# Kernel tuning notes

Hardware: AMD Instinct MI355X
Metric: run time of the kernel (lower is better)

## Reference

```python
import jax, jax.numpy as jnp
import numpy as np

N = 12288
E = 393216
IN_DIM = 256

def _glorot(key, shape):
    lim = float(np.sqrt(6.0 / (shape[0] + shape[1])))
    return jax.random.uniform(key, shape, jnp.float32, -lim, lim)

def setup_inputs() -> dict:
    key = jax.random.key(0)
    ks = jax.random.split(key, 8)
    x = jax.random.normal(ks[0], (N, IN_DIM), jnp.float32)
    edge_index = jax.random.randint(ks[1], (2, E), 0, N, jnp.int64)
    params = {
        'W_e1': _glorot(ks[2], (IN_DIM, 128)), 'b_e1': jnp.zeros((128,), jnp.float32),
        'W_e2': _glorot(ks[3], (128, 64)),     'b_e2': jnp.zeros((64,), jnp.float32),
        'W_a1': _glorot(ks[4], (64, 128)),     'b_a1': jnp.zeros((128,), jnp.float32),
        'W_a2': _glorot(ks[5], (128, IN_DIM)), 'b_a2': jnp.zeros((IN_DIM,), jnp.float32),
        'W_s':  _glorot(ks[6], (64, 64)),      'b_s':  jnp.zeros((64,), jnp.float32),
    }
    return {'x': x, 'edge_index': edge_index, **params}

def _gcn(x, W, b, src, dst, deg_inv, norm):
    # GCNConv: D^{-1/2}(A+I)D^{-1/2} X W + b, self-loops added
    h = x @ W                                   # [N, F_out]
    agg = jax.ops.segment_sum(h[src] * norm[:, None], dst, num_segments=N)
    agg = agg + h * deg_inv[:, None]            # self-loop term (norm = 1/deg)
    return agg + b

def reference(x, edge_index, W_e1, b_e1, W_e2, b_e2, W_a1, b_a1, W_a2, b_a2, W_s, b_s):
    src, dst = edge_index[0], edge_index[1]
    deg = jnp.zeros((N,), jnp.float32).at[dst].add(1.0) + 1.0  # includes self-loop
    dinv_sqrt = jax.lax.rsqrt(deg)
    norm = dinv_sqrt[src] * dinv_sqrt[dst]      # per-edge norm [E]
    deg_inv = 1.0 / deg
    # Encoder
    h = jax.nn.relu(_gcn(x, W_e1, b_e1, src, dst, deg_inv, norm))
    z = jax.nn.relu(_gcn(h, W_e2, b_e2, src, dst, deg_inv, norm))
    # Attribute decoder
    a = jax.nn.relu(_gcn(z, W_a1, b_a1, src, dst, deg_inv, norm))
    x_hat = _gcn(a, W_a2, b_a2, src, dst, deg_inv, norm)
    # Structure decoder
    s = jax.nn.relu(_gcn(z, W_s, b_s, src, dst, deg_inv, norm))
    a_hat = s @ s.T                             # [N, N]
    return (x_hat, a_hat, z)
```

## Files before the change

### kernel.cpp

```cpp
#include <hip/hip_runtime.h>
#include <hip/hip_bf16.h>

#define N_NODES 12288
#define N_EDGES 393216

typedef __attribute__((ext_vector_type(8))) short bf16x8;
typedef __attribute__((ext_vector_type(4))) float f32x4;


__global__ __launch_bounds__(256) void detect_kernel(const unsigned* __restrict__ w,
                                                     unsigned* __restrict__ flag) {
  int i = blockIdx.x * 256 + threadIdx.x;
  unsigned v = w[2 * i + 1];
  unsigned long long b = __ballot(v != 0);
  if ((threadIdx.x & 63) == 0 && b) atomicOr(flag, 1u);
}


__global__ __launch_bounds__(256) void count_kernel(const int* __restrict__ ei,
                                                    const unsigned* __restrict__ flag,
                                                    int* __restrict__ cnt) {
  const bool wide = (*flag == 0);
  int e = blockIdx.x * 256 + threadIdx.x;
  int d = wide ? ei[2 * (N_EDGES + e)] : ei[N_EDGES + e];
  atomicAdd(&cnt[d], 1);
}

__global__ __launch_bounds__(1024) void scan_kernel(const int* __restrict__ cnt,
                                                    int* __restrict__ csr_off,
                                                    int* __restrict__ cursor,
                                                    float* __restrict__ dinv_sqrt,
                                                    float* __restrict__ deg_inv) {
  __shared__ int sdata[1024];
  const int tid = threadIdx.x;
  int carry = 0;
  for (int base = 0; base < N_NODES; base += 1024) {
    int i = base + tid;
    int c = (i < N_NODES) ? cnt[i] : 0;
    if (i < N_NODES) {
      float d = (float)(c + 1);
      dinv_sqrt[i] = rsqrtf(d);
      deg_inv[i] = 1.0f / d;
    }
    sdata[tid] = c;
    __syncthreads();
    for (int off = 1; off < 1024; off <<= 1) {
      int v = (tid >= off) ? sdata[tid - off] : 0;
      __syncthreads();
      sdata[tid] += v;
      __syncthreads();
    }
    int incl = sdata[tid];
    if (i < N_NODES) {
      int excl = carry + incl - c;
      csr_off[i] = excl;
      cursor[i] = excl;
    }
    int total = sdata[1023];
    __syncthreads();
    carry += total;
  }
  if (tid == 0) csr_off[N_NODES] = carry;
}

__global__ __launch_bounds__(256) void scatter_kernel(const int* __restrict__ ei,
                                                      const unsigned* __restrict__ flag,
                                                      const float* __restrict__ dinv_sqrt,
                                                      int* __restrict__ cursor,
                                                      int* __restrict__ csr_src,
                                                      float* __restrict__ csr_w) {
  const bool wide = (*flag == 0);
  int e = blockIdx.x * 256 + threadIdx.x;
  int s = wide ? ei[2 * e] : ei[e];
  int d = wide ? ei[2 * (N_EDGES + e)] : ei[N_EDGES + e];
  int p = atomicAdd(&cursor[d], 1);
  csr_src[p] = s;
  csr_w[p] = dinv_sqrt[s] * dinv_sqrt[d];
}


template <bool BIAS, bool RELU>
__global__ __launch_bounds__(256) void gemm_kernel(const float* __restrict__ A,
                                                   const float* __restrict__ B,
                                                   const float* __restrict__ bias,
                                                   float* __restrict__ C,
                                                   int K, int Nf) {
  __shared__ float As[16][65];
  __shared__ float Bs[16][68];
  const int tid = threadIdx.x;
  const int bm = blockIdx.y * 64;
  const int bn = blockIdx.x * 64;
  const int tr = (tid >> 4) * 4;
  const int tc = (tid & 15) * 4;
  const int lm = tid >> 2;
  const int lk = (tid & 3) * 4;
  const int lbk = tid >> 4;
  const int lbc = (tid & 15) * 4;
  float acc[4][4] = {};
  for (int k0 = 0; k0 < K; k0 += 16) {
    float4 a4 = *reinterpret_cast<const float4*>(&A[(size_t)(bm + lm) * K + k0 + lk]);
    float4 b4 = *reinterpret_cast<const float4*>(&B[(size_t)(k0 + lbk) * Nf + bn + lbc]);
    As[lk + 0][lm] = a4.x; As[lk + 1][lm] = a4.y; As[lk + 2][lm] = a4.z; As[lk + 3][lm] = a4.w;
    Bs[lbk][lbc + 0] = b4.x; Bs[lbk][lbc + 1] = b4.y; Bs[lbk][lbc + 2] = b4.z; Bs[lbk][lbc + 3] = b4.w;
    __syncthreads();
#pragma unroll
    for (int kk = 0; kk < 16; ++kk) {
      float av[4], bv[4];
#pragma unroll
      for (int i = 0; i < 4; ++i) av[i] = As[kk][tr + i];
#pragma unroll
      for (int j = 0; j < 4; ++j) bv[j] = Bs[kk][tc + j];
#pragma unroll
      for (int i = 0; i < 4; ++i)
#pragma unroll
        for (int j = 0; j < 4; ++j) acc[i][j] = fmaf(av[i], bv[j], acc[i][j]);
    }
    __syncthreads();
  }
#pragma unroll
  for (int i = 0; i < 4; ++i) {
    float v[4];
#pragma unroll
    for (int j = 0; j < 4; ++j) {
      float t = acc[i][j];
      if (BIAS) t += bias[bn + tc + j];
      if (RELU) t = fmaxf(t, 0.0f);
      v[j] = t;
    }
    float4 o; o.x = v[0]; o.y = v[1]; o.z = v[2]; o.w = v[3];
    *reinterpret_cast<float4*>(&C[(size_t)(bm + tr + i) * Nf + bn + tc]) = o;
  }
}


template <int F, bool BIAS, bool RELU>
__global__ __launch_bounds__(256) void agg_kernel(const float* __restrict__ H,
                                                  const int* __restrict__ csr_off,
                                                  const int* __restrict__ csr_src,
                                                  const float* __restrict__ csr_w,
                                                  const float* __restrict__ deg_inv,
                                                  const float* __restrict__ bias,
                                                  float* __restrict__ out) {
  constexpr int G = 256 / F;
  const int node = blockIdx.x * G + threadIdx.x / F;
  const int f = threadIdx.x % F;
  const int p0 = csr_off[node];
  const int p1 = csr_off[node + 1];
  float acc = deg_inv[node] * H[(size_t)node * F + f];
  int p = p0;
  for (; p + 1 < p1; p += 2) {
    float w0 = csr_w[p];     int s0 = csr_src[p];
    float w1 = csr_w[p + 1]; int s1 = csr_src[p + 1];
    acc = fmaf(w0, H[(size_t)s0 * F + f], acc);
    acc = fmaf(w1, H[(size_t)s1 * F + f], acc);
  }
  if (p < p1) acc = fmaf(csr_w[p], H[(size_t)csr_src[p] * F + f], acc);
  if (BIAS) acc += bias[f];
  if (RELU) acc = fmaxf(acc, 0.0f);
  out[(size_t)node * F + f] = acc;
}


__device__ __forceinline__ unsigned short f32_to_bf16_rn(float v) {
  unsigned int u = __float_as_uint(v);
  u += 0x7FFFu + ((u >> 16) & 1u);
  return (unsigned short)(u >> 16);
}

__global__ __launch_bounds__(256) void split_kernel(const float* __restrict__ s,
                                                    unsigned short* __restrict__ hi,
                                                    unsigned short* __restrict__ lo) {
  int i = blockIdx.x * 256 + threadIdx.x;
  float v = s[i];
  unsigned short h = f32_to_bf16_rn(v);
  float hf = __uint_as_float(((unsigned int)h) << 16);
  lo[i] = f32_to_bf16_rn(v - hf);
  hi[i] = h;
}


__global__ __launch_bounds__(256) void ahat_kernel(const unsigned short* __restrict__ Shi,
                                                   const unsigned short* __restrict__ Slo,
                                                   float* __restrict__ out) {
  const int lane = threadIdx.x & 63;
  const int wid = threadIdx.x >> 6;
  const int brow = blockIdx.y * 128 + (wid >> 1) * 64;
  const int bcol = blockIdx.x * 128 + (wid & 1) * 64;
  const int r16 = lane & 15;
  const int koff = (lane >> 4) * 8;

  bf16x8 ahi[4][2], alo[4][2], bhi[4][2], blo[4][2];
#pragma unroll
  for (int m = 0; m < 4; ++m) {
#pragma unroll
    for (int ks = 0; ks < 2; ++ks) {
      size_t ai = (size_t)(brow + m * 16 + r16) * 64 + ks * 32 + koff;
      size_t bi = (size_t)(bcol + m * 16 + r16) * 64 + ks * 32 + koff;
      ahi[m][ks] = *reinterpret_cast<const bf16x8*>(&Shi[ai]);
      alo[m][ks] = *reinterpret_cast<const bf16x8*>(&Slo[ai]);
      bhi[m][ks] = *reinterpret_cast<const bf16x8*>(&Shi[bi]);
      blo[m][ks] = *reinterpret_cast<const bf16x8*>(&Slo[bi]);
    }
  }

  f32x4 acc[4][4];
#pragma unroll
  for (int m = 0; m < 4; ++m)
#pragma unroll
    for (int n = 0; n < 4; ++n) acc[m][n] = (f32x4){0.f, 0.f, 0.f, 0.f};

#pragma unroll
  for (int m = 0; m < 4; ++m)
#pragma unroll
    for (int n = 0; n < 4; ++n)
#pragma unroll
      for (int ks = 0; ks < 2; ++ks) {
        acc[m][n] = __builtin_amdgcn_mfma_f32_16x16x32_bf16(ahi[m][ks], bhi[n][ks], acc[m][n], 0, 0, 0);
        acc[m][n] = __builtin_amdgcn_mfma_f32_16x16x32_bf16(ahi[m][ks], blo[n][ks], acc[m][n], 0, 0, 0);
        acc[m][n] = __builtin_amdgcn_mfma_f32_16x16x32_bf16(alo[m][ks], bhi[n][ks], acc[m][n], 0, 0, 0);
      }

  const int crow0 = (lane >> 4) * 4;
#pragma unroll
  for (int m = 0; m < 4; ++m)
#pragma unroll
    for (int n = 0; n < 4; ++n)
#pragma unroll
      for (int r = 0; r < 4; ++r)
        out[(size_t)(brow + m * 16 + crow0 + r) * N_NODES + bcol + n * 16 + r16] = acc[m][n][r];
}


extern "C" void kernel_launch(void* const* d_in, const int* in_sizes, int n_in,
                              void* d_out, int out_size, void* d_ws, size_t ws_size,
                              hipStream_t stream) {
  const float* x    = (const float*)d_in[0];
  const int*   ei   = (const int*)d_in[1];
  const float* W_e1 = (const float*)d_in[2];
  const float* b_e1 = (const float*)d_in[3];
  const float* W_e2 = (const float*)d_in[4];
  const float* b_e2 = (const float*)d_in[5];
  const float* W_a1 = (const float*)d_in[6];
  const float* b_a1 = (const float*)d_in[7];
  const float* W_a2 = (const float*)d_in[8];
  const float* b_a2 = (const float*)d_in[9];
  const float* W_s  = (const float*)d_in[10];
  const float* b_s  = (const float*)d_in[11];

  float* out_xhat = (float*)d_out;
  float* out_ahat = out_xhat + (size_t)N_NODES * 256;
  float* out_z    = out_ahat + (size_t)N_NODES * N_NODES;

  char* scr = (char*)out_ahat;
  size_t o = 0;
  auto alloc = [&](size_t bytes) -> void* {
    void* p = scr + o;
    o = (o + bytes + 255) & ~(size_t)255;
    return p;
  };
  int*   cnt      = (int*)alloc((size_t)N_NODES * 4);
  int*   csr_off  = (int*)alloc((size_t)(N_NODES + 1) * 4);
  int*   cursor   = (int*)alloc((size_t)N_NODES * 4);
  float* dinv     = (float*)alloc((size_t)N_NODES * 4);
  float* deg_inv  = (float*)alloc((size_t)N_NODES * 4);
  int*   csr_src  = (int*)alloc((size_t)N_EDGES * 4);
  float* csr_w    = (float*)alloc((size_t)N_EDGES * 4);
  float* P = (float*)alloc((size_t)N_NODES * 128 * 4);
  float* Q = (float*)alloc((size_t)N_NODES * 128 * 4);
  float* R = (float*)alloc((size_t)N_NODES * 128 * 4);
  float* S = (float*)alloc((size_t)N_NODES * 128 * 4);

  char* ws = (char*)d_ws;
  unsigned short* shi = (unsigned short*)ws;
  unsigned short* slo = shi + (size_t)N_NODES * 64;
  unsigned* eflag = (unsigned*)(slo + (size_t)N_NODES * 64);

  hipMemsetAsync(cnt, 0, (size_t)N_NODES * 4, stream);
  hipMemsetAsync(eflag, 0, 4, stream);
  detect_kernel<<<N_EDGES / 256, 256, 0, stream>>>((const unsigned*)ei, eflag);
  count_kernel<<<N_EDGES / 256, 256, 0, stream>>>(ei, eflag, cnt);
  scan_kernel<<<1, 1024, 0, stream>>>(cnt, csr_off, cursor, dinv, deg_inv);
  scatter_kernel<<<N_EDGES / 256, 256, 0, stream>>>(ei, eflag, dinv, cursor, csr_src, csr_w);

  gemm_kernel<false, false><<<dim3(128 / 64, N_NODES / 64), 256, 0, stream>>>(x, W_e1, nullptr, P, 256, 128);
  agg_kernel<128, true, true><<<N_NODES / 2, 256, 0, stream>>>(P, csr_off, csr_src, csr_w, deg_inv, b_e1, Q);
  gemm_kernel<false, false><<<dim3(64 / 64, N_NODES / 64), 256, 0, stream>>>(Q, W_e2, nullptr, R, 128, 64);
  agg_kernel<64, true, true><<<N_NODES / 4, 256, 0, stream>>>(R, csr_off, csr_src, csr_w, deg_inv, b_e2, out_z);
  agg_kernel<64, false, false><<<N_NODES / 4, 256, 0, stream>>>(out_z, csr_off, csr_src, csr_w, deg_inv, nullptr, P);
  gemm_kernel<true, true><<<dim3(128 / 64, N_NODES / 64), 256, 0, stream>>>(P, W_a1, b_a1, Q, 64, 128);
  gemm_kernel<true, true><<<dim3(64 / 64, N_NODES / 64), 256, 0, stream>>>(P, W_s, b_s, R, 64, 64);
  agg_kernel<128, false, false><<<N_NODES / 2, 256, 0, stream>>>(Q, csr_off, csr_src, csr_w, deg_inv, nullptr, S);
  gemm_kernel<true, false><<<dim3(256 / 64, N_NODES / 64), 256, 0, stream>>>(S, W_a2, b_a2, out_xhat, 128, 256);
  split_kernel<<<(N_NODES * 64) / 256, 256, 0, stream>>>(R, shi, slo);
  ahat_kernel<<<dim3(N_NODES / 128, N_NODES / 128), 256, 0, stream>>>(shi, slo, out_ahat);
}
```

Before: 1.020 ms.

## Fuse bf16 split into GEMM, wave-shuffle scan, swizzle ahat blocks, restructure aggregation

Several changes land together. The bf16 hi/lo split is fused into the W_s GEMM epilogue, which removes a separate split kernel and its extra pass over memory. The single-block scan now uses wavefront shuffles instead of a shared-memory Hillis-Steele loop, and the edge flag moves next to cnt so one memset clears both. The aggregation kernel gets a 2D grid with 64 features per wave and a 4-way unrolled gather for more loads in flight. The ahat kernel remaps block indices with a swizzle to improve L2 locality. The dominant cost is still the large N×N ahat output write, so the combined effect is probably modest.

```diff
diff --git a/kernel.cpp b/kernel.cpp
--- a/kernel.cpp
+++ b/kernel.cpp
@@ -31,34 +31,42 @@
                                                     int* __restrict__ cursor,
                                                     float* __restrict__ dinv_sqrt,
                                                     float* __restrict__ deg_inv) {
-  __shared__ int sdata[1024];
+  __shared__ int wsum[16];
+  __shared__ int wpre[16];
   const int tid = threadIdx.x;
+  const int lane = tid & 63;
+  const int wid = tid >> 6;
   int carry = 0;
   for (int base = 0; base < N_NODES; base += 1024) {
     int i = base + tid;
-    int c = (i < N_NODES) ? cnt[i] : 0;
-    if (i < N_NODES) {
-      float d = (float)(c + 1);
-      dinv_sqrt[i] = rsqrtf(d);
-      deg_inv[i] = 1.0f / d;
-    }
-    sdata[tid] = c;
-    __syncthreads();
-    for (int off = 1; off < 1024; off <<= 1) {
-      int v = (tid >= off) ? sdata[tid - off] : 0;
-      __syncthreads();
-      sdata[tid] += v;
-      __syncthreads();
-    }
-    int incl = sdata[tid];
-    if (i < N_NODES) {
-      int excl = carry + incl - c;
-      csr_off[i] = excl;
-      cursor[i] = excl;
-    }
-    int total = sdata[1023];
-    __syncthreads();
-    carry += total;
+    int c = cnt[i];
+    float dg = (float)(c + 1);
+    dinv_sqrt[i] = rsqrtf(dg);
+    deg_inv[i] = 1.0f / dg;
+    int v = c;
+#pragma unroll
+    for (int d = 1; d < 64; d <<= 1) {
+      int t = __shfl_up(v, d);
+      if (lane >= d) v += t;
+    }
+    if (lane == 63) wsum[wid] = v;
+    __syncthreads();
+    if (tid < 16) {
+      int t = wsum[tid];
+#pragma unroll
+      for (int d = 1; d < 16; d <<= 1) {
+        int u = __shfl_up(t, d);
+        if (tid >= d) t += u;
+      }
+      wpre[tid] = t;
+    }
+    __syncthreads();
+    int incl = carry + (wid ? wpre[wid - 1] : 0) + v;
+    int excl = incl - c;
+    csr_off[i] = excl;
+    cursor[i] = excl;
+    carry += wpre[15];
+    __syncthreads();
   }
   if (tid == 0) csr_off[N_NODES] = carry;
 }
@@ -79,11 +87,20 @@
 }
 
 
-template <bool BIAS, bool RELU>
+__device__ __forceinline__ unsigned short f32_to_bf16_rn(float v) {
+  unsigned int u = __float_as_uint(v);
+  u += 0x7FFFu + ((u >> 16) & 1u);
+  return (unsigned short)(u >> 16);
+}
+
+
+template <bool BIAS, bool RELU, bool SPLIT>
 __global__ __launch_bounds__(256) void gemm_kernel(const float* __restrict__ A,
                                                    const float* __restrict__ B,
                                                    const float* __restrict__ bias,
                                                    float* __restrict__ C,
+                                                   unsigned short* __restrict__ hi,
+                                                   unsigned short* __restrict__ lo,
                                                    int K, int Nf) {
   __shared__ float As[16][65];
   __shared__ float Bs[16][68];
@@ -127,65 +144,78 @@
       if (RELU) t = fmaxf(t, 0.0f);
       v[j] = t;
     }
-    float4 o; o.x = v[0]; o.y = v[1]; o.z = v[2]; o.w = v[3];
-    *reinterpret_cast<float4*>(&C[(size_t)(bm + tr + i) * Nf + bn + tc]) = o;
-  }
-}
-
-
-template <int F, bool BIAS, bool RELU>
+    if (!SPLIT) {
+      float4 o; o.x = v[0]; o.y = v[1]; o.z = v[2]; o.w = v[3];
+      *reinterpret_cast<float4*>(&C[(size_t)(bm + tr + i) * Nf + bn + tc]) = o;
+    } else {
+      ushort4 h4, l4;
+      unsigned short* hp = (unsigned short*)&h4;
+      unsigned short* lp = (unsigned short*)&l4;
+#pragma unroll
+      for (int j = 0; j < 4; ++j) {
+        unsigned short h = f32_to_bf16_rn(v[j]);
+        float hf = __uint_as_float(((unsigned int)h) << 16);
+        hp[j] = h;
+        lp[j] = f32_to_bf16_rn(v[j] - hf);
+      }
+      size_t off = (size_t)(bm + tr + i) * Nf + bn + tc;
+      *reinterpret_cast<ushort4*>(&hi[off]) = h4;
+      *reinterpret_cast<ushort4*>(&lo[off]) = l4;
+    }
+  }
+}
+
+
+template <bool BIAS, bool RELU>
 __global__ __launch_bounds__(256) void agg_kernel(const float* __restrict__ H,
                                                   const int* __restrict__ csr_off,
                                                   const int* __restrict__ csr_src,
                                                   const float* __restrict__ csr_w,
                                                   const float* __restrict__ deg_inv,
                                                   const float* __restrict__ bias,
-                                                  float* __restrict__ out) {
-  constexpr int G = 256 / F;
-  const int node = blockIdx.x * G + threadIdx.x / F;
-  const int f = threadIdx.x % F;
+                                                  float* __restrict__ out,
+                                                  int Fs) {
+  const int node = blockIdx.x * 4 + (threadIdx.x >> 6);
+  const int f = blockIdx.y * 64 + (threadIdx.x & 63);
   const int p0 = csr_off[node];
   const int p1 = csr_off[node + 1];
-  float acc = deg_inv[node] * H[(size_t)node * F + f];
+  float acc = deg_inv[node] * H[(size_t)node * Fs + f];
   int p = p0;
-  for (; p + 1 < p1; p += 2) {
-    float w0 = csr_w[p];     int s0 = csr_src[p];
-    float w1 = csr_w[p + 1]; int s1 = csr_src[p + 1];
-    acc = fmaf(w0, H[(size_t)s0 * F + f], acc);
-    acc = fmaf(w1, H[(size_t)s1 * F + f], acc);
-  }
-  if (p < p1) acc = fmaf(csr_w[p], H[(size_t)csr_src[p] * F + f], acc);
+  for (; p + 3 < p1; p += 4) {
+    int s0 = csr_src[p];     float w0 = csr_w[p];
+    int s1 = csr_src[p + 1]; float w1 = csr_w[p + 1];
+    int s2 = csr_src[p + 2]; float w2 = csr_w[p + 2];
+    int s3 = csr_src[p + 3]; float w3 = csr_w[p + 3];
+    float h0 = H[(size_t)s0 * Fs + f];
+    float h1 = H[(size_t)s1 * Fs + f];
+    float h2 = H[(size_t)s2 * Fs + f];
+    float h3 = H[(size_t)s3 * Fs + f];
+    acc = fmaf(w0, h0, acc);
+    acc = fmaf(w1, h1, acc);
+    acc = fmaf(w2, h2, acc);
+    acc = fmaf(w3, h3, acc);
+  }
+  for (; p < p1; ++p) acc = fmaf(csr_w[p], H[(size_t)csr_src[p] * Fs + f], acc);
   if (BIAS) acc += bias[f];
   if (RELU) acc = fmaxf(acc, 0.0f);
-  out[(size_t)node * F + f] = acc;
-}
-
-
-__device__ __forceinline__ unsigned short f32_to_bf16_rn(float v) {
-  unsigned int u = __float_as_uint(v);
-  u += 0x7FFFu + ((u >> 16) & 1u);
-  return (unsigned short)(u >> 16);
-}
-
-__global__ __launch_bounds__(256) void split_kernel(const float* __restrict__ s,
-                                                    unsigned short* __restrict__ hi,
-                                                    unsigned short* __restrict__ lo) {
-  int i = blockIdx.x * 256 + threadIdx.x;
-  float v = s[i];
-  unsigned short h = f32_to_bf16_rn(v);
-  float hf = __uint_as_float(((unsigned int)h) << 16);
-  lo[i] = f32_to_bf16_rn(v - hf);
-  hi[i] = h;
+  out[(size_t)node * Fs + f] = acc;
 }
 
 
 __global__ __launch_bounds__(256) void ahat_kernel(const unsigned short* __restrict__ Shi,
                                                    const unsigned short* __restrict__ Slo,
                                                    float* __restrict__ out) {
+  const int GW = N_NODES / 128;
+  int flat = blockIdx.y * GW + blockIdx.x;
+  const int NWG = GW * GW;
+  int sw = (flat & 7) * (NWG / 8) + (flat >> 3);
+  const int bx = sw % GW;
+  const int by = sw / GW;
+
   const int lane = threadIdx.x & 63;
   const int wid = threadIdx.x >> 6;
-  const int brow = blockIdx.y * 128 + (wid >> 1) * 64;
-  const int bcol = blockIdx.x * 128 + (wid & 1) * 64;
+  const int brow = by * 128 + (wid >> 1) * 64;
+  const int bcol = bx * 128 + (wid & 1) * 64;
   const int r16 = lane & 15;
   const int koff = (lane >> 4) * 8;
 
@@ -258,7 +288,8 @@
     o = (o + bytes + 255) & ~(size_t)255;
     return p;
   };
-  int*   cnt      = (int*)alloc((size_t)N_NODES * 4);
+  int*   cnt      = (int*)alloc((size_t)(N_NODES + 64) * 4);
+  unsigned* eflag = (unsigned*)(cnt + N_NODES);
   int*   csr_off  = (int*)alloc((size_t)(N_NODES + 1) * 4);
   int*   cursor   = (int*)alloc((size_t)N_NODES * 4);
   float* dinv     = (float*)alloc((size_t)N_NODES * 4);
@@ -273,24 +304,21 @@
   char* ws = (char*)d_ws;
   unsigned short* shi = (unsigned short*)ws;
   unsigned short* slo = shi + (size_t)N_NODES * 64;
-  unsigned* eflag = (unsigned*)(slo + (size_t)N_NODES * 64);
-
-  hipMemsetAsync(cnt, 0, (size_t)N_NODES * 4, stream);
-  hipMemsetAsync(eflag, 0, 4, stream);
+
+  hipMemsetAsync(cnt, 0, (size_t)(N_NODES + 1) * 4, stream);
   detect_kernel<<<N_EDGES / 256, 256, 0, stream>>>((const unsigned*)ei, eflag);
   count_kernel<<<N_EDGES / 256, 256, 0, stream>>>(ei, eflag, cnt);
   scan_kernel<<<1, 1024, 0, stream>>>(cnt, csr_off, cursor, dinv, deg_inv);
   scatter_kernel<<<N_EDGES / 256, 256, 0, stream>>>(ei, eflag, dinv, cursor, csr_src, csr_w);
 
-  gemm_kernel<false, false><<<dim3(128 / 64, N_NODES / 64), 256, 0, stream>>>(x, W_e1, nullptr, P, 256, 128);
-  agg_kernel<128, true, true><<<N_NODES / 2, 256, 0, stream>>>(P, csr_off, csr_src, csr_w, deg_inv, b_e1, Q);
-  gemm_kernel<false, false><<<dim3(64 / 64, N_NODES / 64), 256, 0, stream>>>(Q, W_e2, nullptr, R, 128, 64);
-  agg_kernel<64, true, true><<<N_NODES / 4, 256, 0, stream>>>(R, csr_off, csr_src, csr_w, deg_inv, b_e2, out_z);
-  agg_kernel<64, false, false><<<N_NODES / 4, 256, 0, stream>>>(out_z, csr_off, csr_src, csr_w, deg_inv, nullptr, P);
-  gemm_kernel<true, true><<<dim3(128 / 64, N_NODES / 64), 256, 0, stream>>>(P, W_a1, b_a1, Q, 64, 128);
-  gemm_kernel<true, true><<<dim3(64 / 64, N_NODES / 64), 256, 0, stream>>>(P, W_s, b_s, R, 64, 64);
-  agg_kernel<128, false, false><<<N_NODES / 2, 256, 0, stream>>>(Q, csr_off, csr_src, csr_w, deg_inv, nullptr, S);
-  gemm_kernel<true, false><<<dim3(256 / 64, N_NODES / 64), 256, 0, stream>>>(S, W_a2, b_a2, out_xhat, 128, 256);
-  split_kernel<<<(N_NODES * 64) / 256, 256, 0, stream>>>(R, shi, slo);
+  gemm_kernel<false, false, false><<<dim3(2, 192), 256, 0, stream>>>(x, W_e1, nullptr, P, nullptr, nullptr, 256, 128);
+  agg_kernel<true, true><<<dim3(N_NODES / 4, 2), 256, 0, stream>>>(P, csr_off, csr_src, csr_w, deg_inv, b_e1, Q, 128);
+  gemm_kernel<false, false, false><<<dim3(1, 192), 256, 0, stream>>>(Q, W_e2, nullptr, R, nullptr, nullptr, 128, 64);
+  agg_kernel<true, true><<<dim3(N_NODES / 4, 1), 256, 0, stream>>>(R, csr_off, csr_src, csr_w, deg_inv, b_e2, out_z, 64);
+  agg_kernel<false, false><<<dim3(N_NODES / 4, 1), 256, 0, stream>>>(out_z, csr_off, csr_src, csr_w, deg_inv, nullptr, P, 64);
+  gemm_kernel<true, true, false><<<dim3(2, 192), 256, 0, stream>>>(P, W_a1, b_a1, Q, nullptr, nullptr, 64, 128);
+  gemm_kernel<true, true, true><<<dim3(1, 192), 256, 0, stream>>>(P, W_s, b_s, nullptr, shi, slo, 64, 64);
+  agg_kernel<false, false><<<dim3(N_NODES / 4, 2), 256, 0, stream>>>(Q, csr_off, csr_src, csr_w, deg_inv, nullptr, S, 128);
+  gemm_kernel<true, false, false><<<dim3(4, 192), 256, 0, stream>>>(S, W_a2, b_a2, out_xhat, nullptr, nullptr, 128, 256);
   ahat_kernel<<<dim3(N_NODES / 128, N_NODES / 128), 256, 0, stream>>>(shi, slo, out_ahat);
 }
```

Result: faster. 956.5 us (-6.2%).
